# Optimization experiments

Hardware: AMD Instinct MI355X
Metric: run time of the kernel (lower is better)

Reference implementation:

```python
import jax, jax.numpy as jnp
import numpy as np

B, C, H, W = 8, 21, 512, 512
MAX_M = 0.5   # args.ldam_max_m
S = 30.0      # args.ldam_s


def setup_inputs() -> dict:
    key = jax.random.key(0)
    k1, k2 = jax.random.split(key)
    pred = jax.random.normal(k1, (B, C, H, W), dtype=jnp.float32)
    target = jax.random.randint(k2, (B, H, W), 0, C, dtype=jnp.int32)  # class labels (argmax of one-hot)
    return {"pred": pred, "target": target}


def reference(pred, target):
    labels = target.reshape(-1)  # [N]
    # m_list: per-class pixel counts == sum of one-hot target over (0,2,3)
    counts = jnp.zeros((C,), dtype=pred.dtype).at[labels].add(1.0)
    m_list = 1.0 / jnp.sqrt(jnp.sqrt(counts + 1e-4))
    m_list = m_list * (MAX_M / jnp.max(m_list))

    logits = pred.transpose(0, 2, 3, 1).reshape(-1, C)  # [N, C]
    batch_m = m_list[labels]                            # gather == matmul(m_list, one_hot^T)
    onehot = jax.nn.one_hot(labels, C, dtype=logits.dtype)
    output = logits - batch_m[:, None] * onehot         # subtract margin only at target class

    logp = jax.nn.log_softmax(S * output, axis=-1)
    nll = -jnp.take_along_axis(logp, labels[:, None].astype(jnp.int32), axis=1)[:, 0]
    return jnp.mean(nll)
```

## Files before the change

kernel.cpp:

```cpp
#include <hip/hip_runtime.h>

static constexpr int   Cc  = 21;
static constexpr int   HWn = 512 * 512;
static constexpr int   Nn  = 8 * HWn;
static constexpr float MAXM  = 0.5f;
static constexpr float Sc    = 30.0f;
static constexpr float LOG2E = 1.4426950408889634f;
static constexpr float LN2   = 0.6931471805599453f;

static constexpr int HIST_BLOCKS = 512;
static constexpr int LOSS_BLOCKS = Nn / 4 / 256;

static constexpr int WS_COUNTS = 0;
static constexpr int WS_FLAG   = 96;
static constexpr int WS_SM     = 128;
static constexpr int WS_PART   = 256;

__global__ __launch_bounds__(256) void hist_kernel(const int4* __restrict__ t4,
                                                   int* __restrict__ counts) {
    __shared__ int lh[4][Cc];
    int t = threadIdx.x;
    if (t < 4 * Cc) ((int*)lh)[t] = 0;
    __syncthreads();
    int wave = t >> 6;
    int base = blockIdx.x * (256 * 4) + t;
    #pragma unroll
    for (int i = 0; i < 4; ++i) {
        int4 v = t4[base + i * 256];
        atomicAdd(&lh[wave][v.x], 1);
        atomicAdd(&lh[wave][v.y], 1);
        atomicAdd(&lh[wave][v.z], 1);
        atomicAdd(&lh[wave][v.w], 1);
    }
    __syncthreads();
    if (t < Cc)
        atomicAdd(&counts[t], lh[0][t] + lh[1][t] + lh[2][t] + lh[3][t]);
}

__global__ __launch_bounds__(64) void mlist_kernel(const int* __restrict__ counts,
                                                   float* __restrict__ sm2) {
    int t = threadIdx.x;
    float mval = 0.0f;
    if (t < Cc) {
        float cnt = (float)counts[t] + 1e-4f;
        mval = 1.0f / sqrtf(sqrtf(cnt));
    }
    float mx = mval;
    #pragma unroll
    for (int o = 32; o >= 1; o >>= 1) mx = fmaxf(mx, __shfl_down(mx, o));
    mx = __shfl(mx, 0);
    if (t < Cc) sm2[t] = Sc * LOG2E * mval * (MAXM / mx);
}

__global__ __launch_bounds__(256, 2) void loss_kernel(const float* __restrict__ pred,
                                                      const int4* __restrict__ t4,
                                                      const float* __restrict__ smg,
                                                      double* __restrict__ partial,
                                                      unsigned int* __restrict__ flag,
                                                      float* __restrict__ out) {
    __shared__ float  s_sm[Cc];
    __shared__ float  wsum[4];
    __shared__ double dsum[4];
    __shared__ bool   s_last;
    int t = threadIdx.x;
    if (t < Cc) s_sm[t] = smg[t];
    __syncthreads();

    int tid = blockIdx.x * 256 + t;
    int n0  = tid * 4;
    int b   = n0 >> 18;
    int hw  = n0 & (HWn - 1);
    const float4* p4 = (const float4*)(pred + (size_t)b * Cc * HWn + hw);

    float4 x[Cc];
    #pragma unroll
    for (int c = 0; c < Cc; ++c) x[c] = p4[(size_t)c * (HWn / 4)];

    int4 y4 = t4[tid];
    int ys[4] = {y4.x, y4.y, y4.z, y4.w};
    float smy[4];
    #pragma unroll
    for (int k = 0; k < 4; ++k) smy[k] = s_sm[ys[k]];

    const float S2 = Sc * LOG2E;

    float mx[4] = {-1e30f, -1e30f, -1e30f, -1e30f};
    float vy[4] = {0.f, 0.f, 0.f, 0.f};
    #pragma unroll
    for (int c = 0; c < Cc; ++c) {
        float xs[4] = {x[c].x, x[c].y, x[c].z, x[c].w};
        #pragma unroll
        for (int k = 0; k < 4; ++k) {
            bool  isy = (c == ys[k]);
            float val = fmaf(S2, xs[k], isy ? -smy[k] : 0.0f);
            mx[k] = fmaxf(mx[k], val);
            vy[k] = isy ? val : vy[k];
        }
    }

    float nll2 = 0.0f;
    #pragma unroll
    for (int k = 0; k < 4; ++k) {
        float cb = -mx[k];
        float cy = -smy[k] - mx[k];
        float sum = 0.0f;
        #pragma unroll
        for (int c = 0; c < Cc; ++c) {
            float xs = (k == 0) ? x[c].x : (k == 1) ? x[c].y : (k == 2) ? x[c].z : x[c].w;
            sum += exp2f(fmaf(S2, xs, (c == ys[k]) ? cy : cb));
        }
        nll2 += __log2f(sum) + mx[k] - vy[k];
    }
    float nll = nll2 * LN2;

    #pragma unroll
    for (int o = 32; o >= 1; o >>= 1) nll += __shfl_down(nll, o);

    int wave = t >> 6;
    int lane = t & 63;
    if (lane == 0) wsum[wave] = nll;
    __syncthreads();
    if (t == 0) {
        float bsum = wsum[0] + wsum[1] + wsum[2] + wsum[3];
        partial[blockIdx.x] = (double)bsum;
        __threadfence();
        unsigned done = atomicAdd(flag, 1u);
        s_last = (done == (unsigned)(LOSS_BLOCKS - 1));
    }
    __syncthreads();

    if (s_last) {
        __threadfence();
        double sm = 0.0;
        for (int i = t; i < LOSS_BLOCKS; i += 256) sm += partial[i];
        #pragma unroll
        for (int o = 32; o >= 1; o >>= 1) sm += __shfl_down(sm, o);
        if ((t & 63) == 0) dsum[t >> 6] = sm;
        __syncthreads();
        if (t == 0)
            out[0] = (float)((dsum[0] + dsum[1] + dsum[2] + dsum[3]) / (double)Nn);
    }
}

extern "C" void kernel_launch(void* const* d_in, const int* in_sizes, int n_in,
                              void* d_out, int out_size, void* d_ws, size_t ws_size,
                              hipStream_t stream) {
    const float* pred   = (const float*)d_in[0];
    const int*   target = (const int*)d_in[1];
    float*       out    = (float*)d_out;

    char* ws = (char*)d_ws;
    int*          counts  = (int*)(ws + WS_COUNTS);
    unsigned int* flag    = (unsigned int*)(ws + WS_FLAG);
    float*        sm      = (float*)(ws + WS_SM);
    double*       partial = (double*)(ws + WS_PART);

    hipMemsetAsync(d_ws, 0, 128, stream);

    hist_kernel <<<HIST_BLOCKS, 256, 0, stream>>>((const int4*)target, counts);
    mlist_kernel<<<1,           64,  0, stream>>>(counts, sm);
    loss_kernel <<<LOSS_BLOCKS, 256, 0, stream>>>(pred, (const int4*)target, sm,
                                                  partial, flag, out);
}
```

Measured before the change: 328.4 us.

## Stream classes with online softmax and double-buffered loads, 16 pixels per thread

```diff
diff --git a/kernel.cpp b/kernel.cpp
--- a/kernel.cpp
+++ b/kernel.cpp
@@ -9,7 +9,7 @@
 static constexpr float LN2   = 0.6931471805599453f;
 
 static constexpr int HIST_BLOCKS = 512;
-static constexpr int LOSS_BLOCKS = Nn / 4 / 256;
+static constexpr int LOSS_BLOCKS = 512;
 
 static constexpr int WS_COUNTS = 0;
 static constexpr int WS_FLAG   = 96;
@@ -52,8 +52,18 @@
     if (t < Cc) sm2[t] = Sc * LOG2E * mval * (MAXM / mx);
 }
 
+__device__ __forceinline__ void upd1(float x, int y, float smy, int c, float S2,
+                                     float& m, float& s, float& v) {
+    bool  isy = (c == y);
+    float val = fmaf(S2, x, isy ? -smy : 0.0f);
+    float mn  = fmaxf(m, val);
+    s = fmaf(s, exp2f(m - mn), exp2f(val - mn));
+    v = isy ? val : v;
+    m = mn;
+}
+
 __global__ __launch_bounds__(256, 2) void loss_kernel(const float* __restrict__ pred,
-                                                      const int4* __restrict__ t4,
+                                                      const int* __restrict__ target,
                                                       const float* __restrict__ smg,
                                                       double* __restrict__ partial,
                                                       unsigned int* __restrict__ flag,
@@ -66,58 +76,63 @@
     if (t < Cc) s_sm[t] = smg[t];
     __syncthreads();
 
-    int tid = blockIdx.x * 256 + t;
-    int n0  = tid * 4;
-    int b   = n0 >> 18;
-    int hw  = n0 & (HWn - 1);
-    const float4* p4 = (const float4*)(pred + (size_t)b * Cc * HWn + hw);
+    int wave = t >> 6;
+    int lane = t & 63;
+    int gw   = blockIdx.x * 4 + wave;
+    int P0   = gw << 10;
+    int b    = P0 >> 18;
+    int hw0  = P0 & (HWn - 1);
+    int poff = lane * 4;
+    const float* base = pred + (size_t)b * (Cc * HWn) + hw0;
 
-    float4 x[Cc];
+    float xm[16], xs[16], xv[16], xsm[16];
+    int   xy[16];
     #pragma unroll
-    for (int c = 0; c < Cc; ++c) x[c] = p4[(size_t)c * (HWn / 4)];
-
-    int4 y4 = t4[tid];
-    int ys[4] = {y4.x, y4.y, y4.z, y4.w};
-    float smy[4];
+    for (int j = 0; j < 4; ++j) {
+        int4 yv = *(const int4*)&target[P0 + j * 256 + poff];
+        xy[4 * j + 0] = yv.x;  xsm[4 * j + 0] = s_sm[yv.x];
+        xy[4 * j + 1] = yv.y;  xsm[4 * j + 1] = s_sm[yv.y];
+        xy[4 * j + 2] = yv.z;  xsm[4 * j + 2] = s_sm[yv.z];
+        xy[4 * j + 3] = yv.w;  xsm[4 * j + 3] = s_sm[yv.w];
+    }
     #pragma unroll
-    for (int k = 0; k < 4; ++k) smy[k] = s_sm[ys[k]];
+    for (int i = 0; i < 16; ++i) { xm[i] = -1e30f; xs[i] = 0.0f; xv[i] = 0.0f; }
 
     const float S2 = Sc * LOG2E;
+    float4 bufA[4], bufB[4];
 
-    float mx[4] = {-1e30f, -1e30f, -1e30f, -1e30f};
-    float vy[4] = {0.f, 0.f, 0.f, 0.f};
+#define LOADB_(B, c) { const float* pc_ = base + (size_t)(c) * HWn + poff;      \
+        B[0] = *(const float4*)(pc_);        B[1] = *(const float4*)(pc_ + 256);\
+        B[2] = *(const float4*)(pc_ + 512);  B[3] = *(const float4*)(pc_ + 768); }
+#define UPD4_(B, J, c)                                                              \
+        upd1(B[J].x, xy[4*(J)+0], xsm[4*(J)+0], (c), S2, xm[4*(J)+0], xs[4*(J)+0], xv[4*(J)+0]); \
+        upd1(B[J].y, xy[4*(J)+1], xsm[4*(J)+1], (c), S2, xm[4*(J)+1], xs[4*(J)+1], xv[4*(J)+1]); \
+        upd1(B[J].z, xy[4*(J)+2], xsm[4*(J)+2], (c), S2, xm[4*(J)+2], xs[4*(J)+2], xv[4*(J)+2]); \
+        upd1(B[J].w, xy[4*(J)+3], xsm[4*(J)+3], (c), S2, xm[4*(J)+3], xs[4*(J)+3], xv[4*(J)+3]);
+#define PROC_(B, c) { UPD4_(B, 0, c) UPD4_(B, 1, c) UPD4_(B, 2, c) UPD4_(B, 3, c) }
+
+    LOADB_(bufA, 0);
+    #pragma unroll 1
+    for (int c = 0; c < 20; c += 2) {
+        LOADB_(bufB, c + 1);
+        PROC_(bufA, c);
+        LOADB_(bufA, c + 2);
+        PROC_(bufB, c + 1);
+    }
+    PROC_(bufA, 20);
+
+#undef LOADB_
+#undef UPD4_
+#undef PROC_
+
+    float nll = 0.0f;
     #pragma unroll
-    for (int c = 0; c < Cc; ++c) {
-        float xs[4] = {x[c].x, x[c].y, x[c].z, x[c].w};
-        #pragma unroll
-        for (int k = 0; k < 4; ++k) {
-            bool  isy = (c == ys[k]);
-            float val = fmaf(S2, xs[k], isy ? -smy[k] : 0.0f);
-            mx[k] = fmaxf(mx[k], val);
-            vy[k] = isy ? val : vy[k];
-        }
-    }
-
-    float nll2 = 0.0f;
-    #pragma unroll
-    for (int k = 0; k < 4; ++k) {
-        float cb = -mx[k];
-        float cy = -smy[k] - mx[k];
-        float sum = 0.0f;
-        #pragma unroll
-        for (int c = 0; c < Cc; ++c) {
-            float xs = (k == 0) ? x[c].x : (k == 1) ? x[c].y : (k == 2) ? x[c].z : x[c].w;
-            sum += exp2f(fmaf(S2, xs, (c == ys[k]) ? cy : cb));
-        }
-        nll2 += __log2f(sum) + mx[k] - vy[k];
-    }
-    float nll = nll2 * LN2;
+    for (int i = 0; i < 16; ++i) nll += __log2f(xs[i]) + xm[i] - xv[i];
+    nll *= LN2;
 
     #pragma unroll
     for (int o = 32; o >= 1; o >>= 1) nll += __shfl_down(nll, o);
 
-    int wave = t >> 6;
-    int lane = t & 63;
     if (lane == 0) wsum[wave] = nll;
     __syncthreads();
     if (t == 0) {
@@ -159,6 +174,6 @@
 
     hist_kernel <<<HIST_BLOCKS, 256, 0, stream>>>((const int4*)target, counts);
     mlist_kernel<<<1,           64,  0, stream>>>(counts, sm);
-    loss_kernel <<<LOSS_BLOCKS, 256, 0, stream>>>(pred, (const int4*)target, sm,
+    loss_kernel <<<LOSS_BLOCKS, 256, 0, stream>>>(pred, target, sm,
                                                   partial, flag, out);
 }
```

Measured after the change: 274.3 us. -16.5%, faster.
